# Kernel tuning notes

Hardware: AMD Instinct MI355X
Metric: run time of the kernel (lower is better)

The kernel has to match this reference:

```python
import jax, jax.numpy as jnp
import numpy as np

B, S, E, H = 2, 2048, 1024, 16
D = E // H  # head_dim = 64


def setup_inputs() -> dict:
    key = jax.random.key(0)
    ks = jax.random.split(key, 5)
    return {
        "hidden_states": jax.random.normal(ks[0], (B, S, E), jnp.float32),
        "c_attn_w": jax.random.normal(ks[1], (E, 3 * E), jnp.float32) * 0.02,
        "c_attn_b": jnp.zeros((3 * E,), jnp.float32),
        "c_proj_w": jax.random.normal(ks[2], (E, E), jnp.float32) * 0.02,
        "c_proj_b": jnp.zeros((E,), jnp.float32),
    }


def reference(hidden_states, c_attn_w, c_attn_b, c_proj_w, c_proj_b):
    # Conv1D: x @ w + b -> qkv [B, S, 3E]
    qkv = hidden_states @ c_attn_w + c_attn_b
    q, k, v = jnp.split(qkv, 3, axis=-1)
    # [B, H, S, D]
    q = q.reshape(B, S, H, D).transpose(0, 2, 1, 3)
    k = k.reshape(B, S, H, D).transpose(0, 2, 1, 3)
    v = v.reshape(B, S, H, D).transpose(0, 2, 1, 3)
    # scores [B, H, S, S], scaled by sqrt(head_dim)
    scores = jnp.einsum("bhqd,bhkd->bhqk", q, k) / jnp.sqrt(jnp.asarray(D, q.dtype))
    causal = jnp.tril(jnp.ones((S, S), bool))  # [S, S]
    mask_value = jnp.finfo(scores.dtype).min
    scores = jnp.where(causal, scores, mask_value)
    attn = jax.nn.softmax(scores, axis=-1)
    # attn @ V -> [B, H, S, D] -> [B, S, E]
    out = jnp.einsum("bhqk,bhkd->bhqd", attn, v)
    out = out.transpose(0, 2, 1, 3).reshape(B, S, E)
    return out @ c_proj_w + c_proj_b
```

## Files before the change

### kernel.cpp

```cpp
#include <hip/hip_runtime.h>

using bf16 = __bf16;
typedef __bf16 bf16x8 __attribute__((ext_vector_type(8)));
typedef __bf16 bf16x4 __attribute__((ext_vector_type(4)));
typedef float  f32x4  __attribute__((ext_vector_type(4)));

#define MFMA16(a, b, c) __builtin_amdgcn_mfma_f32_16x16x32_bf16((a), (b), (c), 0, 0, 0)

static constexpr int S = 2048, E = 1024;
static constexpr float CSCALE = 0.18033688011112042f;

__device__ __forceinline__ void gld16(const bf16* g, bf16* l) {
    __builtin_amdgcn_global_load_lds((const __attribute__((address_space(1))) unsigned*)g,
                                     (__attribute__((address_space(3))) unsigned*)l, 16, 0, 0);
}

__global__ __launch_bounds__(256) void k_prep(const float* __restrict__ hs, const float* __restrict__ w0,
                                              const float* __restrict__ w1, bf16* __restrict__ A0,
                                              bf16* __restrict__ Wt0, bf16* __restrict__ Wt1) {
    __shared__ float tile[32][33];
    const int bx = blockIdx.x;
    if (bx < 4096) {
        int i = (bx * 256 + threadIdx.x) * 4;
        float4 v = *(const float4*)(hs + i);
        bf16x4 o = { (bf16)v.x, (bf16)v.y, (bf16)v.z, (bf16)v.w };
        *(bf16x4*)(A0 + i) = o;
        return;
    }
    const float* in;
    bf16* outp;
    int K, N, nb, kb;
    if (bx < 4096 + 3072) {
        int j = bx - 4096; in = w0; outp = Wt0; K = 1024; N = 3072; nb = j % 96; kb = j / 96;
    } else {
        int j = bx - 7168; in = w1; outp = Wt1; K = 1024; N = 1024; nb = j % 32; kb = j / 32;
    }
    const int bxx = nb * 32, byy = kb * 32;
    const int tx = threadIdx.x & 31, ty = threadIdx.x >> 5;
#pragma unroll
    for (int i = 0; i < 32; i += 8)
        tile[ty + i][tx] = in[(long)(byy + ty + i) * N + bxx + tx];
    __syncthreads();
#pragma unroll
    for (int i = 0; i < 32; i += 8)
        outp[(long)(bxx + ty + i) * K + byy + tx] = (bf16)tile[tx][ty + i];
}

__global__ __launch_bounds__(256) void k_gemm_qkv(const bf16* __restrict__ A, const bf16* __restrict__ Bt,
                                                  const float* __restrict__ bias, bf16* __restrict__ Qs,
                                                  bf16* __restrict__ Kf, bf16* __restrict__ Vf, int Kk) {
    const int bm = blockIdx.x * 128;
    const int bn = blockIdx.y * 128;
    const int tid = threadIdx.x;
    const int w = tid >> 6, lane = tid & 63;
    const int wm = (w >> 1) * 64, wn = (w & 1) * 64;
    const int col = lane & 15, quad = lane >> 4;

    __shared__ __align__(16) char smem[32768];
    bf16* sA = (bf16*)smem;
    bf16* sB = (bf16*)(smem + 16384);
    bf16* T  = (bf16*)smem;

    const bf16* pA[4]; const bf16* pB[4]; bf16* lA[4]; bf16* lB[4];
#pragma unroll
    for (int i = 0; i < 4; i++) {
        const int c = i * 256 + w * 64 + lane;
        const int r = c >> 3, sl = (c & 7) ^ (r & 7);
        pA[i] = A  + (long)(bm + r) * Kk + sl * 8;
        pB[i] = Bt + (long)(bn + r) * Kk + sl * 8;
        lA[i] = sA + i * 2048 + w * 512;
        lB[i] = sB + i * 2048 + w * 512;
    }

    f32x4 acc[4][4] = {};

    for (int k0 = 0; k0 < Kk; k0 += 64) {
        __syncthreads();
#pragma unroll
        for (int i = 0; i < 4; i++) gld16(pA[i] + k0, lA[i]);
#pragma unroll
        for (int i = 0; i < 4; i++) gld16(pB[i] + k0, lB[i]);
        __syncthreads();
#pragma unroll
        for (int h = 0; h < 2; h++) {
            bf16x8 af[4], bfr[4];
#pragma unroll
            for (int mt = 0; mt < 4; mt++) {
                const int row = wm + mt * 16 + col;
                af[mt] = *(const bf16x8*)(sA + row * 64 + (((h * 4 + quad) ^ (col & 7)) * 8));
            }
#pragma unroll
            for (int nt = 0; nt < 4; nt++) {
                const int row = wn + nt * 16 + col;
                bfr[nt] = *(const bf16x8*)(sB + row * 64 + (((h * 4 + quad) ^ (col & 7)) * 8));
            }
#pragma unroll
            for (int mt = 0; mt < 4; mt++)
#pragma unroll
                for (int nt = 0; nt < 4; nt++)
                    acc[mt][nt] = MFMA16(af[mt], bfr[nt], acc[mt][nt]);
        }
    }

    const int seg = bn >> 10;
    const int b = bm >> 11;
    const int kt0 = (bm & 2047) >> 6;

    if (seg == 0) {
#pragma unroll
        for (int mt = 0; mt < 4; mt++) {
            const int gr = bm + wm + mt * 16 + quad * 4;
#pragma unroll
            for (int nt = 0; nt < 4; nt++) {
                const int gc = bn + wn + nt * 16 + col;
                const float bv = bias[gc];
#pragma unroll
                for (int r = 0; r < 4; r++)
                    Qs[(long)(gr + r) * 1024 + gc] = (bf16)((acc[mt][nt][r] + bv) * CSCALE);
            }
        }
        return;
    }

    const int hl = w >> 1;
    if (seg == 1) {
        const int bh = b * 16 + (bn >> 6) - 16 + hl;
#pragma unroll 1
        for (int p = 0; p < 2; p++) {
            __syncthreads();
            if ((wm >> 6) == p) {
#pragma unroll
                for (int mt = 0; mt < 4; mt++) {
                    const int sl = mt * 16 + quad * 4;
#pragma unroll
                    for (int nt = 0; nt < 4; nt++) {
                        const int gcl = wn + nt * 16 + col;
                        const float bv = bias[bn + gcl];
#pragma unroll
                        for (int r = 0; r < 4; r++)
                            T[(sl + r) * 136 + gcl] = (bf16)(acc[mt][nt][r] + bv);
                    }
                }
            }
            __syncthreads();
            const int ktp = kt0 + p;
#pragma unroll
            for (int mi = 0; mi < 2; mi++) {
                const int mt = (w & 1) * 2 + mi;
#pragma unroll
                for (int half = 0; half < 2; half++) {
                    bf16x8 ch = *(const bf16x8*)(T + (mt * 16 + col) * 136 + hl * 64 + half * 32 + quad * 8);
                    const long chunk = ((long)(bh * 32 + ktp) * 8 + mt * 2 + half) * 64 + lane;
                    *(bf16x8*)(Kf + chunk * 8) = ch;
                }
            }
        }
    } else {
        const int bh = b * 16 + (bn >> 6) - 32 + hl;
#pragma unroll 1
        for (int p = 0; p < 2; p++) {
            __syncthreads();
            if ((wm >> 6) == p) {
#pragma unroll
                for (int mt = 0; mt < 4; mt++) {
                    const int sl = mt * 16 + quad * 4;
#pragma unroll
                    for (int nt = 0; nt < 4; nt++) {
                        const int gcl = wn + nt * 16 + col;
                        const float bv = bias[bn + gcl];
                        bf16x4 pk = { (bf16)(acc[mt][nt][0] + bv), (bf16)(acc[mt][nt][1] + bv),
                                      (bf16)(acc[mt][nt][2] + bv), (bf16)(acc[mt][nt][3] + bv) };
                        *(bf16x4*)(T + gcl * 72 + sl) = pk;
                    }
                }
            }
            __syncthreads();
            const int ktp = kt0 + p;
#pragma unroll
            for (int di = 0; di < 2; di++) {
                const int dt = (w & 1) * 2 + di;
#pragma unroll
                for (int ks = 0; ks < 2; ks++) {
                    bf16x8 ch = *(const bf16x8*)(T + (hl * 64 + dt * 16 + col) * 72 + ks * 32 + quad * 8);
                    const long chunk = ((long)(bh * 32 + ktp) * 8 + dt * 2 + ks) * 64 + lane;
                    *(bf16x8*)(Vf + chunk * 8) = ch;
                }
            }
        }
    }
}

__global__ __launch_bounds__(256) void k_gemm_bt64(const bf16* __restrict__ A, const bf16* __restrict__ Bt,
                                                    const float* __restrict__ bias, float* __restrict__ Cout,
                                                    int Mm, int Nn, int Kk) {
    const int bm = blockIdx.x * 64;
    const int bn = blockIdx.y * 128;
    const int tid = threadIdx.x;
    const int w = tid >> 6, lane = tid & 63;
    const int wm = (w >> 1) * 32, wn = (w & 1) * 64;
    const int col = lane & 15, quad = lane >> 4;

    __shared__ bf16 sA[64 * 64];
    __shared__ bf16 sB[128 * 64];

    const bf16* pA[2]; bf16* lA[2];
#pragma unroll
    for (int i = 0; i < 2; i++) {
        const int c = i * 256 + w * 64 + lane;
        const int r = c >> 3, sl = (c & 7) ^ (r & 7);
        pA[i] = A + (long)(bm + r) * Kk + sl * 8;
        lA[i] = sA + i * 2048 + w * 512;
    }
    const bf16* pB[4]; bf16* lB[4];
#pragma unroll
    for (int i = 0; i < 4; i++) {
        const int c = i * 256 + w * 64 + lane;
        const int r = c >> 3, sl = (c & 7) ^ (r & 7);
        pB[i] = Bt + (long)(bn + r) * Kk + sl * 8;
        lB[i] = sB + i * 2048 + w * 512;
    }

    f32x4 acc[2][4] = {};

    for (int k0 = 0; k0 < Kk; k0 += 64) {
        __syncthreads();
#pragma unroll
        for (int i = 0; i < 2; i++) gld16(pA[i] + k0, lA[i]);
#pragma unroll
        for (int i = 0; i < 4; i++) gld16(pB[i] + k0, lB[i]);
        __syncthreads();
#pragma unroll
        for (int h = 0; h < 2; h++) {
            bf16x8 af[2], bfr[4];
#pragma unroll
            for (int mt = 0; mt < 2; mt++) {
                const int row = wm + mt * 16 + col;
                af[mt] = *(const bf16x8*)(sA + row * 64 + (((h * 4 + quad) ^ (col & 7)) * 8));
            }
#pragma unroll
            for (int nt = 0; nt < 4; nt++) {
                const int row = wn + nt * 16 + col;
                bfr[nt] = *(const bf16x8*)(sB + row * 64 + (((h * 4 + quad) ^ (col & 7)) * 8));
            }
#pragma unroll
            for (int mt = 0; mt < 2; mt++)
#pragma unroll
                for (int nt = 0; nt < 4; nt++)
                    acc[mt][nt] = MFMA16(af[mt], bfr[nt], acc[mt][nt]);
        }
    }

#pragma unroll
    for (int mt = 0; mt < 2; mt++) {
        const int gr = bm + wm + mt * 16 + quad * 4;
#pragma unroll
        for (int nt = 0; nt < 4; nt++) {
            const int gc = bn + wn + nt * 16 + col;
            const float bv = bias[gc];
#pragma unroll
            for (int r = 0; r < 4; r++)
                Cout[(long)(gr + r) * Nn + gc] = acc[mt][nt][r] + bv;
        }
    }
}

__global__ __launch_bounds__(128) void k_attn(const bf16* __restrict__ Qs, const bf16* __restrict__ Kf,
                                              const bf16* __restrict__ Vf, bf16* __restrict__ out) {
    const int bh = blockIdx.x & 31;
    const int tp = blockIdx.x >> 5;
    const int b = bh >> 4, h = bh & 15;
    const int tid = threadIdx.x;
    const int w = tid >> 6, lane = tid & 63;
    const int col = lane & 15, quad = lane >> 4;

    __shared__ bf16 sP[2][32 * 72];
    __shared__ float M[2][64][36];
    bf16* pw = sP[w];

    const bf16* kfb = Kf + ((long)bh << 17) + lane * 8;
    const bf16* vfb = Vf + ((long)bh << 17) + lane * 8;

#pragma unroll 1
    for (int sel = 0; sel < 2; sel++) {
        const int t = sel ? 63 - tp : tp;
        const int q0 = t * 32;
        const int nkt = (t >> 1) + 1;
        const int kA = nkt >> 1;
        const int kbeg = w ? kA : 0;
        const int kend = w ? nkt : kA;

        bf16x8 bq[2][2];
#pragma unroll
        for (int qg = 0; qg < 2; qg++) {
            const bf16* qp = Qs + (long)(b * S + q0 + qg * 16 + col) * E + h * 64 + quad * 8;
            bq[qg][0] = *(const bf16x8*)(qp);
            bq[qg][1] = *(const bf16x8*)(qp + 32);
        }
        float m_[2] = { -1e30f, -1e30f }, l_[2] = { 0.f, 0.f };
        f32x4 o[2][4] = {};

#pragma unroll 1
        for (int kt = kbeg; kt < kend; kt++) {
            bf16x8 kfr[4][2], vfr[4][2];
#pragma unroll
            for (int mt = 0; mt < 4; mt++)
#pragma unroll
                for (int half = 0; half < 2; half++)
                    kfr[mt][half] = *(const bf16x8*)(kfb + ((long)(kt * 8 + mt * 2 + half) << 9));
#pragma unroll
            for (int dt = 0; dt < 4; dt++)
#pragma unroll
                for (int ks = 0; ks < 2; ks++)
                    vfr[dt][ks] = *(const bf16x8*)(vfb + ((long)(kt * 8 + dt * 2 + ks) << 9));

            f32x4 s[2][4];
#pragma unroll
            for (int mt = 0; mt < 4; mt++)
#pragma unroll
                for (int qg = 0; qg < 2; qg++) {
                    f32x4 z = {};
                    z = MFMA16(kfr[mt][0], bq[qg][0], z);
                    z = MFMA16(kfr[mt][1], bq[qg][1], z);
                    s[qg][mt] = z;
                }
            if (kt == nkt - 1) {
#pragma unroll
                for (int qg = 0; qg < 2; qg++) {
                    const int qrow = q0 + qg * 16 + col;
#pragma unroll
                    for (int mt = 0; mt < 4; mt++)
#pragma unroll
                        for (int r = 0; r < 4; r++)
                            if (kt * 64 + mt * 16 + quad * 4 + r > qrow) s[qg][mt][r] = -1e30f;
                }
            }
#pragma unroll
            for (int qg = 0; qg < 2; qg++) {
                float cm = -1e30f;
#pragma unroll
                for (int mt = 0; mt < 4; mt++)
#pragma unroll
                    for (int r = 0; r < 4; r++) cm = fmaxf(cm, s[qg][mt][r]);
                cm = fmaxf(cm, __shfl_xor(cm, 16));
                cm = fmaxf(cm, __shfl_xor(cm, 32));
                const float mnew = fmaxf(m_[qg], cm);
                const float alpha = __builtin_amdgcn_exp2f(m_[qg] - mnew);
                m_[qg] = mnew;
                float rs = 0.f;
#pragma unroll
                for (int mt = 0; mt < 4; mt++)
#pragma unroll
                    for (int r = 0; r < 4; r++) {
                        float pe = __builtin_amdgcn_exp2f(s[qg][mt][r] - mnew);
                        s[qg][mt][r] = pe;
                        rs += pe;
                    }
                l_[qg] = l_[qg] * alpha + rs;
#pragma unroll
                for (int dt = 0; dt < 4; dt++)
#pragma unroll
                    for (int r = 0; r < 4; r++) o[qg][dt][r] *= alpha;
#pragma unroll
                for (int mt = 0; mt < 4; mt++) {
                    bf16x4 pk = { (bf16)s[qg][mt][0], (bf16)s[qg][mt][1],
                                  (bf16)s[qg][mt][2], (bf16)s[qg][mt][3] };
                    *(bf16x4*)(pw + (qg * 16 + col) * 72 + mt * 16 + quad * 4) = pk;
                }
            }
#pragma unroll
            for (int ks = 0; ks < 2; ks++) {
                bf16x8 ap[2];
#pragma unroll
                for (int qg = 0; qg < 2; qg++)
                    ap[qg] = *(const bf16x8*)(pw + (qg * 16 + col) * 72 + ks * 32 + quad * 8);
#pragma unroll
                for (int dt = 0; dt < 4; dt++)
#pragma unroll
                    for (int qg = 0; qg < 2; qg++)
                        o[qg][dt] = MFMA16(vfr[dt][ks], ap[qg], o[qg][dt]);
            }
        }

#pragma unroll
        for (int qg = 0; qg < 2; qg++) {
            float lt = l_[qg];
            lt += __shfl_xor(lt, 16);
            lt += __shfl_xor(lt, 32);
            l_[qg] = lt;
        }

        if (w == 0) {
#pragma unroll
            for (int qg = 0; qg < 2; qg++) {
#pragma unroll
                for (int dt = 0; dt < 4; dt++)
                    *(f32x4*)&M[sel][lane][qg * 16 + dt * 4] = o[qg][dt];
                M[sel][lane][32 + qg * 2] = m_[qg];
                M[sel][lane][33 + qg * 2] = l_[qg];
            }
        }
        __syncthreads();
        if (w == 1) {
#pragma unroll
            for (int qg = 0; qg < 2; qg++) {
                const float m0 = M[sel][lane][32 + qg * 2];
                const float l0 = M[sel][lane][33 + qg * 2];
                const float mm = fmaxf(m0, m_[qg]);
                const float a0 = __builtin_amdgcn_exp2f(m0 - mm);
                const float a1 = __builtin_amdgcn_exp2f(m_[qg] - mm);
                const float li = 1.f / (l0 * a0 + l_[qg] * a1);
                bf16* op = out + (long)(b * S + q0 + qg * 16 + col) * E + h * 64 + quad * 4;
#pragma unroll
                for (int dt = 0; dt < 4; dt++) {
                    f32x4 o0 = *(const f32x4*)&M[sel][lane][qg * 16 + dt * 4];
                    bf16x4 ov;
#pragma unroll
                    for (int r = 0; r < 4; r++)
                        ov[r] = (bf16)((o0[r] * a0 + o[qg][dt][r] * a1) * li);
                    *(bf16x4*)(op + dt * 16) = ov;
                }
            }
        }
    }
}

extern "C" void kernel_launch(void* const* d_in, const int* in_sizes, int n_in,
                              void* d_out, int out_size, void* d_ws, size_t ws_size,
                              hipStream_t stream) {
    const float* hs = (const float*)d_in[0];
    const float* w0 = (const float*)d_in[1];
    const float* b0 = (const float*)d_in[2];
    const float* w1 = (const float*)d_in[3];
    const float* b1 = (const float*)d_in[4];
    float* outp = (float*)d_out;

    char* ws = (char*)d_ws;
    bf16* A0    = (bf16*)(ws);
    bf16* Wt0   = (bf16*)(ws + 8388608);
    bf16* Wt1   = (bf16*)(ws + 14680064);
    bf16* Qs    = (bf16*)(ws + 16777216);
    bf16* Kf    = (bf16*)(ws + 25165824);
    bf16* Vf    = (bf16*)(ws + 33554432);
    bf16* attnO = (bf16*)(ws + 41943040);

    k_prep<<<8192, 256, 0, stream>>>(hs, w0, w1, A0, Wt0, Wt1);
    k_gemm_qkv<<<dim3(32, 24), 256, 0, stream>>>(A0, Wt0, b0, Qs, Kf, Vf, 1024);
    k_attn<<<1024, 128, 0, stream>>>(Qs, Kf, Vf, attnO);
    k_gemm_bt64<<<dim3(64, 8), 256, 0, stream>>>(attnO, Wt1, b1, outp, 4096, 1024, 1024);
}
```

Measured before the change: 178.1 us.

## Rewrite QKV GEMM with 256x256 tiles, 4-stage LDS pipeline and XCD swizzle

The QKV projection GEMM moves from 128x128 tiles with a single-buffered, sync-heavy loop to 256x256 tiles computed by 512 threads. A 4-stage global_load_lds ring buffer keeps loads in flight, and the A and B loads are split around two MFMA phases with s_setprio. Block IDs are remapped so neighbouring tiles land on the same XCD, and the K/V epilogue uses per-wave LDS scratch with no block barriers. The goal is to hide memory latency and raise MFMA utilisation, at the cost of 128KB LDS per block, heavy register pressure, and only 192 blocks to fill the GPU.

Measured after the change: 172.8 us. -3.0%, faster.

```diff
diff --git a/kernel.cpp b/kernel.cpp
--- a/kernel.cpp
+++ b/kernel.cpp
@@ -46,146 +46,177 @@
         outp[(long)(bxx + ty + i) * K + byy + tx] = (bf16)tile[tx][ty + i];
 }
 
-__global__ __launch_bounds__(256) void k_gemm_qkv(const bf16* __restrict__ A, const bf16* __restrict__ Bt,
-                                                  const float* __restrict__ bias, bf16* __restrict__ Qs,
-                                                  bf16* __restrict__ Kf, bf16* __restrict__ Vf, int Kk) {
-    const int bm = blockIdx.x * 128;
-    const int bn = blockIdx.y * 128;
+__global__ __launch_bounds__(512, 2) void k_gemm_qkv(const bf16* __restrict__ A, const bf16* __restrict__ Bt,
+                                                     const float* __restrict__ bias, bf16* __restrict__ Qs,
+                                                     bf16* __restrict__ Kf, bf16* __restrict__ Vf, int Kk) {
+    __shared__ __align__(16) char smem[131072];
+    bf16* sA = (bf16*)smem;
+    bf16* sB = (bf16*)(smem + 65536);
+
+    const int NT = Kk >> 5;
+
+    const int cpx = gridDim.x >> 3;
+    const int bid = blockIdx.x;
+    const int sid = (bid & 7) * cpx + (bid >> 3);
+    const long bm = (long)(sid & 15) * 256;
+    const int bnT = sid >> 4;
+    const long bn = (long)bnT * 256;
+
     const int tid = threadIdx.x;
     const int w = tid >> 6, lane = tid & 63;
-    const int wm = (w >> 1) * 64, wn = (w & 1) * 64;
     const int col = lane & 15, quad = lane >> 4;
-
-    __shared__ __align__(16) char smem[32768];
-    bf16* sA = (bf16*)smem;
-    bf16* sB = (bf16*)(smem + 16384);
-    bf16* T  = (bf16*)smem;
-
-    const bf16* pA[4]; const bf16* pB[4]; bf16* lA[4]; bf16* lB[4];
-#pragma unroll
-    for (int i = 0; i < 4; i++) {
-        const int c = i * 256 + w * 64 + lane;
-        const int r = c >> 3, sl = (c & 7) ^ (r & 7);
-        pA[i] = A  + (long)(bm + r) * Kk + sl * 8;
-        pB[i] = Bt + (long)(bn + r) * Kk + sl * 8;
-        lA[i] = sA + i * 2048 + w * 512;
-        lB[i] = sB + i * 2048 + w * 512;
-    }
-
-    f32x4 acc[4][4] = {};
-
-    for (int k0 = 0; k0 < Kk; k0 += 64) {
-        __syncthreads();
-#pragma unroll
-        for (int i = 0; i < 4; i++) gld16(pA[i] + k0, lA[i]);
-#pragma unroll
-        for (int i = 0; i < 4; i++) gld16(pB[i] + k0, lB[i]);
-        __syncthreads();
-#pragma unroll
-        for (int h = 0; h < 2; h++) {
-            bf16x8 af[4], bfr[4];
-#pragma unroll
-            for (int mt = 0; mt < 4; mt++) {
-                const int row = wm + mt * 16 + col;
-                af[mt] = *(const bf16x8*)(sA + row * 64 + (((h * 4 + quad) ^ (col & 7)) * 8));
-            }
-#pragma unroll
-            for (int nt = 0; nt < 4; nt++) {
-                const int row = wn + nt * 16 + col;
-                bfr[nt] = *(const bf16x8*)(sB + row * 64 + (((h * 4 + quad) ^ (col & 7)) * 8));
-            }
-#pragma unroll
-            for (int mt = 0; mt < 4; mt++)
-#pragma unroll
-                for (int nt = 0; nt < 4; nt++)
-                    acc[mt][nt] = MFMA16(af[mt], bfr[nt], acc[mt][nt]);
-        }
-    }
-
-    const int seg = bn >> 10;
-    const int b = bm >> 11;
-    const int kt0 = (bm & 2047) >> 6;
+    const int wr = w >> 2, wc = w & 3;
+    const int wrow = wr * 128, wcol = wc * 64;
+
+    const int c0 = tid, c1 = 512 + tid;
+    const int r0 = c0 >> 2, g0 = (c0 & 3) ^ ((r0 >> 1) & 3);
+    const int r1 = c1 >> 2, g1 = (c1 & 3) ^ ((r1 >> 1) & 3);
+    const bf16* gA0 = A + (bm + r0) * Kk + g0 * 8;
+    const bf16* gA1 = A + (bm + r1) * Kk + g1 * 8;
+    const bf16* gB0 = Bt + (bn + r0) * Kk + g0 * 8;
+    const bf16* gB1 = Bt + (bn + r1) * Kk + g1 * 8;
+
+    f32x4 acc[8][4] = {};
+
+#pragma unroll
+    for (int tt = 0; tt < 3; ++tt) {
+        bf16* dA = sA + tt * 8192;
+        bf16* dB = sB + tt * 8192;
+        gld16(gA0 + tt * 32, dA + w * 512);
+        gld16(gA1 + tt * 32, dA + 4096 + w * 512);
+        gld16(gB0 + tt * 32, dB + w * 512);
+        gld16(gB1 + tt * 32, dB + 4096 + w * 512);
+    }
+    asm volatile("s_waitcnt vmcnt(8)" ::: "memory");
+    __builtin_amdgcn_s_barrier();
+
+#pragma unroll 1
+    for (int t = 0; t < NT; ++t) {
+        const bf16* sAs = sA + (t & 3) * 8192;
+        const bf16* sBs = sB + (t & 3) * 8192;
+        const int ts = t + 3;
+        bf16* dA = sA + (ts & 3) * 8192;
+        bf16* dB = sB + (ts & 3) * 8192;
+
+        bf16x8 bfr[4], af[4];
+#pragma unroll
+        for (int nt = 0; nt < 4; ++nt) {
+            const int row = wcol + nt * 16 + col;
+            bfr[nt] = *(const bf16x8*)(sBs + row * 32 + ((quad ^ ((row >> 1) & 3)) * 8));
+        }
+#pragma unroll
+        for (int mt = 0; mt < 4; ++mt) {
+            const int row = wrow + mt * 16 + col;
+            af[mt] = *(const bf16x8*)(sAs + row * 32 + ((quad ^ ((row >> 1) & 3)) * 8));
+        }
+        if (ts < NT) {
+            gld16(gA0 + ts * 32, dA + w * 512);
+            gld16(gA1 + ts * 32, dA + 4096 + w * 512);
+        }
+        __builtin_amdgcn_s_barrier();
+        __builtin_amdgcn_s_setprio(1);
+#pragma unroll
+        for (int mt = 0; mt < 4; ++mt)
+#pragma unroll
+            for (int nt = 0; nt < 4; ++nt)
+                acc[mt][nt] = MFMA16(af[mt], bfr[nt], acc[mt][nt]);
+        __builtin_amdgcn_s_setprio(0);
+        __builtin_amdgcn_s_barrier();
+
+#pragma unroll
+        for (int mt = 0; mt < 4; ++mt) {
+            const int row = wrow + 64 + mt * 16 + col;
+            af[mt] = *(const bf16x8*)(sAs + row * 32 + ((quad ^ ((row >> 1) & 3)) * 8));
+        }
+        if (ts < NT) {
+            gld16(gB0 + ts * 32, dB + w * 512);
+            gld16(gB1 + ts * 32, dB + 4096 + w * 512);
+        }
+        __builtin_amdgcn_s_barrier();
+        __builtin_amdgcn_s_setprio(1);
+#pragma unroll
+        for (int mt = 0; mt < 4; ++mt)
+#pragma unroll
+            for (int nt = 0; nt < 4; ++nt)
+                acc[4 + mt][nt] = MFMA16(af[mt], bfr[nt], acc[4 + mt][nt]);
+        __builtin_amdgcn_s_setprio(0);
+        if (t < NT - 3)       asm volatile("s_waitcnt vmcnt(8)" ::: "memory");
+        else if (t == NT - 3) asm volatile("s_waitcnt vmcnt(4)" ::: "memory");
+        else if (t == NT - 2) asm volatile("s_waitcnt vmcnt(0)" ::: "memory");
+        __builtin_amdgcn_s_barrier();
+    }
+
+    const int seg = bnT >> 2;
 
     if (seg == 0) {
 #pragma unroll
-        for (int mt = 0; mt < 4; mt++) {
-            const int gr = bm + wm + mt * 16 + quad * 4;
-#pragma unroll
-            for (int nt = 0; nt < 4; nt++) {
-                const int gc = bn + wn + nt * 16 + col;
-                const float bv = bias[gc];
-#pragma unroll
-                for (int r = 0; r < 4; r++)
-                    Qs[(long)(gr + r) * 1024 + gc] = (bf16)((acc[mt][nt][r] + bv) * CSCALE);
+        for (int nt = 0; nt < 4; ++nt) {
+            const long gc = bn + wcol + nt * 16 + col;
+            const float bv = bias[gc];
+#pragma unroll
+            for (int mt = 0; mt < 8; ++mt) {
+                const long gr = bm + wrow + mt * 16 + quad * 4;
+#pragma unroll
+                for (int r = 0; r < 4; ++r)
+                    Qs[(gr + r) * 1024 + gc] = (bf16)((acc[mt][nt][r] + bv) * CSCALE);
             }
         }
         return;
     }
 
-    const int hl = w >> 1;
+    bf16* myT = (bf16*)smem + w * (64 * 72);
+    const int bmi = (int)bm;
+    const int b = bmi >> 11;
+    const int ktw = ((bmi & 2047) >> 6) + wr * 2;
+    float bv[4];
+#pragma unroll
+    for (int nt = 0; nt < 4; ++nt) bv[nt] = bias[bn + wcol + nt * 16 + col];
+
     if (seg == 1) {
-        const int bh = b * 16 + (bn >> 6) - 16 + hl;
-#pragma unroll 1
-        for (int p = 0; p < 2; p++) {
-            __syncthreads();
-            if ((wm >> 6) == p) {
-#pragma unroll
-                for (int mt = 0; mt < 4; mt++) {
-                    const int sl = mt * 16 + quad * 4;
-#pragma unroll
-                    for (int nt = 0; nt < 4; nt++) {
-                        const int gcl = wn + nt * 16 + col;
-                        const float bv = bias[bn + gcl];
-#pragma unroll
-                        for (int r = 0; r < 4; r++)
-                            T[(sl + r) * 136 + gcl] = (bf16)(acc[mt][nt][r] + bv);
-                    }
-                }
-            }
-            __syncthreads();
-            const int ktp = kt0 + p;
-#pragma unroll
-            for (int mi = 0; mi < 2; mi++) {
-                const int mt = (w & 1) * 2 + mi;
-#pragma unroll
-                for (int half = 0; half < 2; half++) {
-                    bf16x8 ch = *(const bf16x8*)(T + (mt * 16 + col) * 136 + hl * 64 + half * 32 + quad * 8);
-                    const long chunk = ((long)(bh * 32 + ktp) * 8 + mt * 2 + half) * 64 + lane;
+        const int head = (((int)bn - 1024) >> 6) + wc;
+        const int bh = b * 16 + head;
+#pragma unroll
+        for (int p = 0; p < 2; ++p) {
+#pragma unroll
+            for (int mt2 = 0; mt2 < 4; ++mt2)
+#pragma unroll
+                for (int nt = 0; nt < 4; ++nt)
+#pragma unroll
+                    for (int r = 0; r < 4; ++r)
+                        myT[(mt2 * 16 + quad * 4 + r) * 72 + nt * 16 + col] =
+                            (bf16)(acc[p * 4 + mt2][nt][r] + bv[nt]);
+#pragma unroll
+            for (int mtp = 0; mtp < 4; ++mtp)
+#pragma unroll
+                for (int half = 0; half < 2; ++half) {
+                    bf16x8 ch = *(const bf16x8*)(myT + (mtp * 16 + col) * 72 + half * 32 + quad * 8);
+                    const long chunk = ((long)(bh * 32 + ktw + p) * 8 + mtp * 2 + half) * 64 + lane;
                     *(bf16x8*)(Kf + chunk * 8) = ch;
                 }
-            }
         }
     } else {
-        const int bh = b * 16 + (bn >> 6) - 32 + hl;
-#pragma unroll 1
-        for (int p = 0; p < 2; p++) {
-            __syncthreads();
-            if ((wm >> 6) == p) {
-#pragma unroll
-                for (int mt = 0; mt < 4; mt++) {
-                    const int sl = mt * 16 + quad * 4;
-#pragma unroll
-                    for (int nt = 0; nt < 4; nt++) {
-                        const int gcl = wn + nt * 16 + col;
-                        const float bv = bias[bn + gcl];
-                        bf16x4 pk = { (bf16)(acc[mt][nt][0] + bv), (bf16)(acc[mt][nt][1] + bv),
-                                      (bf16)(acc[mt][nt][2] + bv), (bf16)(acc[mt][nt][3] + bv) };
-                        *(bf16x4*)(T + gcl * 72 + sl) = pk;
-                    }
-                }
-            }
-            __syncthreads();
-            const int ktp = kt0 + p;
-#pragma unroll
-            for (int di = 0; di < 2; di++) {
-                const int dt = (w & 1) * 2 + di;
-#pragma unroll
-                for (int ks = 0; ks < 2; ks++) {
-                    bf16x8 ch = *(const bf16x8*)(T + (hl * 64 + dt * 16 + col) * 72 + ks * 32 + quad * 8);
-                    const long chunk = ((long)(bh * 32 + ktp) * 8 + dt * 2 + ks) * 64 + lane;
+        const int head = (((int)bn - 2048) >> 6) + wc;
+        const int bh = b * 16 + head;
+#pragma unroll
+        for (int p = 0; p < 2; ++p) {
+#pragma unroll
+            for (int nt = 0; nt < 4; ++nt)
+#pragma unroll
+                for (int mt2 = 0; mt2 < 4; ++mt2) {
+                    bf16x4 pk = { (bf16)(acc[p * 4 + mt2][nt][0] + bv[nt]),
+                                  (bf16)(acc[p * 4 + mt2][nt][1] + bv[nt]),
+                                  (bf16)(acc[p * 4 + mt2][nt][2] + bv[nt]),
+                                  (bf16)(acc[p * 4 + mt2][nt][3] + bv[nt]) };
+                    *(bf16x4*)(myT + (nt * 16 + col) * 72 + mt2 * 16 + quad * 4) = pk;
+                }
+#pragma unroll
+            for (int dt = 0; dt < 4; ++dt)
+#pragma unroll
+                for (int ks = 0; ks < 2; ++ks) {
+                    bf16x8 ch = *(const bf16x8*)(myT + (dt * 16 + col) * 72 + ks * 32 + quad * 8);
+                    const long chunk = ((long)(bh * 32 + ktw + p) * 8 + dt * 2 + ks) * 64 + lane;
                     *(bf16x8*)(Vf + chunk * 8) = ch;
                 }
-            }
         }
     }
 }
@@ -444,7 +475,7 @@
     bf16* attnO = (bf16*)(ws + 41943040);
 
     k_prep<<<8192, 256, 0, stream>>>(hs, w0, w1, A0, Wt0, Wt1);
-    k_gemm_qkv<<<dim3(32, 24), 256, 0, stream>>>(A0, Wt0, b0, Qs, Kf, Vf, 1024);
+    k_gemm_qkv<<<192, 512, 0, stream>>>(A0, Wt0, b0, Qs, Kf, Vf, 1024);
     k_attn<<<1024, 128, 0, stream>>>(Qs, Kf, Vf, attnO);
     k_gemm_bt64<<<dim3(64, 8), 256, 0, stream>>>(attnO, Wt1, b1, outp, 4096, 1024, 1024);
 }
```
